# Optimization experiments

Measured on AMD Instinct MI355X. Metric: run time of the kernel, lower is better.

Reference implementation:

```python
import jax, jax.numpy as jnp
import numpy as np

EPS = 1e-6

def setup_inputs() -> dict:
    key = jax.random.key(0)
    ks = jax.random.split(key, 12)
    B, C, H, W = 2, 192, 192, 192
    f = lambda k, s, sc=1.0: jax.random.normal(k, s, dtype=jnp.float32) * sc
    d = {}
    d["x_l"] = f(ks[0], (B, C, H, W))
    d["x_r"] = f(ks[1], (B, C, H, W))
    d["ln_l_w"] = jnp.ones((C,), jnp.float32)
    d["ln_l_b"] = jnp.zeros((C,), jnp.float32)
    d["ln_r_w"] = jnp.ones((C,), jnp.float32)
    d["ln_r_b"] = jnp.zeros((C,), jnp.float32)
    s = C ** -0.5
    d["wq_l"] = f(ks[2], (C, C), s)   # 1x1 conv weights as [out,in]
    d["wq_r"] = f(ks[3], (C, C), s)
    d["wv_l"] = f(ks[4], (C, C), s)
    d["wv_r"] = f(ks[5], (C, C), s)
    d["mlp_w1"] = f(ks[6], (C // 24, C // 3), (C // 3) ** -0.5)
    d["mlp_w2"] = f(ks[7], (C * 2 // 3, C // 24), (C // 24) ** -0.5)
    d["scale_h"] = jnp.ones((1,), jnp.float32)
    d["scale_w"] = jnp.ones((1,), jnp.float32)
    # layer scales are zero-init in the module; use small random so output is nontrivial
    d["ls1"] = f(ks[8], (1, C, 1, 1), 0.1)
    d["ls2"] = f(ks[9], (1, C, 1, 1), 0.1)
    return d

def _ln2d(x, w, b):
    # LayerNorm over channel dim of NCHW
    mu = x.mean(1, keepdims=True)
    var = ((x - mu) ** 2).mean(1, keepdims=True)
    return (x - mu) * jax.lax.rsqrt(var + EPS) * w[None, :, None, None] + b[None, :, None, None]

def _pw(x, w):
    # 1x1 conv, no bias
    return jnp.einsum('bchw,oc->bohw', x, w)

def reference(x_l, x_r, ln_l_w, ln_l_b, ln_r_w, ln_r_b, wq_l, wq_r, wv_l, wv_r,
              mlp_w1, mlp_w2, scale_h, scale_w, ls1, ls2):
    q_l_h, q_l_w, q_l_c = jnp.split(_pw(_ln2d(x_l, ln_l_w, ln_l_b), wq_l), 3, axis=1)
    q_r_h, q_r_w, q_r_c = jnp.split(_pw(_ln2d(x_r, ln_r_w, ln_r_b), wq_r), 3, axis=1)
    v_l_h, v_l_w, v_l_c = jnp.split(_pw(x_l, wv_l), 3, axis=1)
    v_r_h, v_r_w, v_r_c = jnp.split(_pw(x_r, wv_r), 3, axis=1)

    # height axial attention: scores [b, w, h, h']
    attn_h = jnp.einsum('bchw,bcgw->bwhg', q_l_h, q_r_h) * scale_h[0]
    attn_h = jax.nn.softmax(attn_h, axis=-1)
    x_r2l_h = jnp.einsum('bwhg,bcgw->bchw', attn_h, v_r_h)           # [b,c,h,w]
    x_l2r_h = jnp.einsum('bwhg,bchw->bcgw', attn_h, v_l_h)           # attn^T @ v_l

    # width axial attention: scores [b, h, w, w'] (softmax applied separately per direction)
    attn_w = jnp.einsum('bchw,bchv->bhwv', q_l_w, q_r_w) * scale_w[0]
    a1 = jax.nn.softmax(attn_w, axis=-1)
    x_r2l_w = jnp.einsum('bhwv,bchv->bchw', a1, v_r_w)
    a2 = jax.nn.softmax(jnp.swapaxes(attn_w, -1, -2), axis=-1)       # [b,h,v,w]
    x_l2r_w = jnp.einsum('bhvw,bchw->bchv', a2, v_l_w)

    # channel SE branch: sum of the two channel queries, GAP, bottleneck MLP
    p = (q_l_c + q_r_c).mean(axis=(2, 3))                            # [b, c]
    h1 = jax.nn.relu(p @ mlp_w1.T)                                   # [b, c//8]
    a = jax.nn.softmax(h1 @ mlp_w2.T, axis=1)                        # softmax over 2c channels jointly
    attn_l_c, attn_r_c = jnp.split(a, 2, axis=1)
    x_r2l_c = attn_l_c[:, :, None, None] * v_l_c
    x_l2r_c = attn_r_c[:, :, None, None] * v_r_c

    x_r2l = jnp.concatenate([x_r2l_h, x_r2l_w, x_r2l_c], axis=1)
    x_l2r = jnp.concatenate([x_l2r_h, x_l2r_w, x_l2r_c], axis=1)
    out_l = x_r2l * ls1 + x_l
    out_r = x_l2r * ls2 + x_r
    return (out_l, out_r)
```

## Files before the change

kernel.cpp:

```cpp
#include <hip/hip_runtime.h>
#include <stdint.h>

#define NN 36864
#define PL 7077888
#define PL64 2359296
#define TOT 14155776

typedef unsigned short ushort_t;
typedef __attribute__((ext_vector_type(8))) __bf16 bf16x8;
typedef __attribute__((ext_vector_type(4))) float f32x4;
typedef __attribute__((ext_vector_type(4))) unsigned int u32x4;
typedef __attribute__((ext_vector_type(2))) unsigned int u32x2;

__device__ __forceinline__ ushort_t f2bf(float f) {
  unsigned int u = __builtin_bit_cast(unsigned int, f);
  u = (u + 0x7FFFu + ((u >> 16) & 1u)) >> 16;
  return (ushort_t)u;
}
__device__ __forceinline__ float bf2f(ushort_t h) {
  unsigned int u = ((unsigned int)h) << 16;
  return __builtin_bit_cast(float, u);
}
__device__ __forceinline__ bf16x8 lds8(const ushort_t* p) {
  return __builtin_bit_cast(bf16x8, *(const u32x4*)p);
}
__device__ __forceinline__ f32x4 mfma16(bf16x8 a, bf16x8 b, f32x4 c) {
  return __builtin_amdgcn_mfma_f32_16x16x32_bf16(a, b, c, 0, 0, 0);
}
__device__ __forceinline__ unsigned cvtpk(float lo, float hi) {
  unsigned r;
  asm("v_cvt_pk_bf16_f32 %0, %1, %2" : "=v"(r) : "v"(lo), "v"(hi));
  return r;
}

__global__ void k_prep(const float* __restrict__ wq, const float* __restrict__ wv,
                       const float* __restrict__ lnw, const float* __restrict__ lnb,
                       ushort_t* __restrict__ W, float* __restrict__ ab) {
  __shared__ float sa[3], sb[3];
  int r = blockIdx.x, t = threadIdx.x;
  if (r < 192) {
    float w  = wq[r*192 + t];
    float lw = lnw[t], lb = lnb[t];
    W[r*192 + t] = f2bf(w * lw);
    float av = w * lb, bv = -w * lw;
    #pragma unroll
    for (int off = 1; off < 64; off <<= 1) {
      av += __shfl_xor(av, off);
      bv += __shfl_xor(bv, off);
    }
    if ((t & 63) == 0) { sa[t >> 6] = av; sb[t >> 6] = bv; }
    __syncthreads();
    if (t == 0) { ab[r] = sa[0]+sa[1]+sa[2]; ab[192 + r] = sb[0]+sb[1]+sb[2]; }
  } else {
    W[r*192 + t] = f2bf(wv[(r-192)*192 + t]);
  }
}

__global__ __launch_bounds__(512, 2) void k_proj(
    const float* __restrict__ xl, const float* __restrict__ xr,
    const ushort_t* __restrict__ Wl, const ushort_t* __restrict__ Wr,
    const float* __restrict__ abl, const float* __restrict__ abr,
    ushort_t* __restrict__ qhTl, ushort_t* __restrict__ qhTr,
    ushort_t* __restrict__ qwTl, ushort_t* __restrict__ qwTr,
    ushort_t* __restrict__ Vl, ushort_t* __restrict__ Vr,
    float* __restrict__ gpart) {
  __shared__ union {
    struct { ushort_t A[2][4096]; ushort_t B[2][6144]; } kl;
    struct { ushort_t T[192*72]; float gsum[64]; } ep;
  } sm;
  __shared__ float spart[4][192], spart2[4][192];
  __shared__ float smu[192], srs[192];

  const int side = blockIdx.y;
  const float*    x  = side ? xr  : xl;
  const ushort_t* W  = side ? Wr  : Wl;
  const float*    ab = side ? abr : abl;
  ushort_t* qhT = side ? qhTr : qhTl;
  ushort_t* qwT = side ? qwTr : qwTl;
  ushort_t* V   = side ? Vr   : Vl;

  const int bx = blockIdx.x;
  const int mb = bx % 3;
  const int bh = bx / 3;
  const int b  = bh / 192, h = bh % 192;
  const int m0 = mb * 128;
  const int tid = threadIdx.x;
  const int wave = tid >> 6, lane = tid & 63, lr = lane & 15, lg = lane >> 4;
  const int wm = wave >> 2, wn = wave & 3;

  const int kg0 = tid / 192, n_0 = tid - kg0 * 192;
  const int id1 = 512 + (tid & 255);
  const int kg1 = id1 / 192, n_1 = id1 - kg1 * 192;
  const float* xb0 = x + (size_t)b*PL + (size_t)(kg0*8)*NN + h*192 + n_0;
  const float* xb1 = x + (size_t)b*PL + (size_t)(kg1*8)*NN + h*192 + n_1;
  const int bw0 = n_0*32 + 8*(kg0 ^ ((n_0 >> 1) & 3));
  const int bw1 = n_1*32 + 8*(kg1 ^ ((n_1 >> 1) & 3));
  const int am = tid >> 2, akb = tid & 3;
  const ushort_t* wsrc = W + (m0 + am)*192 + akb*8;
  const int aw = am*32 + 8*(akb ^ ((am >> 1) & 3));
  const int slotR = 8 * (lg ^ ((lr >> 1) & 3));

  const f32x4 fz = {0.f, 0.f, 0.f, 0.f};
  f32x4 acc[4][3];
  #pragma unroll
  for (int mf = 0; mf < 4; ++mf)
    #pragma unroll
    for (int nf = 0; nf < 3; ++nf) acc[mf][nf] = fz;

  float sA0 = 0.f, sB0 = 0.f, sA1 = 0.f, sB1 = 0.f;

  {
    u32x4 aV = *(const u32x4*)wsrc;
    float g0[8], g1[8];
    #pragma unroll
    for (int j = 0; j < 8; ++j) g0[j] = xb0[(size_t)j*NN];
    if (tid < 256) {
      #pragma unroll
      for (int j = 0; j < 8; ++j) g1[j] = xb1[(size_t)j*NN];
    }
    *(u32x4*)&sm.kl.A[0][aw] = aV;
    union { ushort_t us[8]; u32x4 v; } t0;
    #pragma unroll
    for (int j = 0; j < 8; ++j) { t0.us[j] = f2bf(g0[j]); sA0 += g0[j]; sB0 += g0[j]*g0[j]; }
    *(u32x4*)&sm.kl.B[0][bw0] = t0.v;
    if (tid < 256) {
      union { ushort_t us[8]; u32x4 v; } t1;
      #pragma unroll
      for (int j = 0; j < 8; ++j) { t1.us[j] = f2bf(g1[j]); sA1 += g1[j]; sB1 += g1[j]*g1[j]; }
      *(u32x4*)&sm.kl.B[0][bw1] = t1.v;
    }
  }
  __syncthreads();

  for (int ks = 0; ks < 6; ++ks) {
    const int cur = ks & 1, nxt = cur ^ 1;
    u32x4 aN;
    float g0[8], g1[8];
    if (ks < 5) {
      const int k0n = (ks + 1) * 32;
      aN = *(const u32x4*)(wsrc + k0n);
      #pragma unroll
      for (int j = 0; j < 8; ++j) g0[j] = xb0[(size_t)(k0n + j)*NN];
      if (tid < 256) {
        #pragma unroll
        for (int j = 0; j < 8; ++j) g1[j] = xb1[(size_t)(k0n + j)*NN];
      }
    }
    bf16x8 bfr[3];
    #pragma unroll
    for (int nf = 0; nf < 3; ++nf)
      bfr[nf] = lds8(&sm.kl.B[cur][(wn*48 + nf*16 + lr)*32 + slotR]);
    #pragma unroll
    for (int mf = 0; mf < 4; ++mf) {
      bf16x8 af = lds8(&sm.kl.A[cur][(wm*64 + mf*16 + lr)*32 + slotR]);
      #pragma unroll
      for (int nf = 0; nf < 3; ++nf) acc[mf][nf] = mfma16(af, bfr[nf], acc[mf][nf]);
    }
    if (ks < 5) {
      *(u32x4*)&sm.kl.A[nxt][aw] = aN;
      union { ushort_t us[8]; u32x4 v; } t0;
      #pragma unroll
      for (int j = 0; j < 8; ++j) { t0.us[j] = f2bf(g0[j]); sA0 += g0[j]; sB0 += g0[j]*g0[j]; }
      *(u32x4*)&sm.kl.B[nxt][bw0] = t0.v;
      if (tid < 256) {
        union { ushort_t us[8]; u32x4 v; } t1;
        #pragma unroll
        for (int j = 0; j < 8; ++j) { t1.us[j] = f2bf(g1[j]); sA1 += g1[j]; sB1 += g1[j]*g1[j]; }
        *(u32x4*)&sm.kl.B[nxt][bw1] = t1.v;
      }
    }
    __syncthreads();
  }

  spart[kg0][n_0] = sA0; spart2[kg0][n_0] = sB0;
  if (tid < 256) { spart[kg1][n_1] = sA1; spart2[kg1][n_1] = sB1; }
  if (mb == 1 && tid >= 448) sm.ep.gsum[tid - 448] = 0.f;
  __syncthreads();
  if (tid < 192) {
    float s  = spart[0][tid] + spart[1][tid] + spart[2][tid] + spart[3][tid];
    float s2 = spart2[0][tid] + spart2[1][tid] + spart2[2][tid] + spart2[3][tid];
    float mu = s * (1.f/192.f);
    float var = s2 * (1.f/192.f) - mu*mu;
    smu[tid] = mu;
    srs[tid] = rsqrtf(var + 1e-6f);
  }
  __syncthreads();

  if (mb == 0) {
    float rst[3], mrs[3];
    #pragma unroll
    for (int nf = 0; nf < 3; ++nf) {
      int n_ = wn*48 + nf*16 + lr;
      float rs = srs[n_];
      rst[nf] = rs;
      mrs[nf] = smu[n_] * rs;
    }
    #pragma unroll
    for (int mf = 0; mf < 4; ++mf) {
      #pragma unroll
      for (int i = 0; i < 4; ++i) {
        int m = wm*64 + mf*16 + lg*4 + i;
        float a_ = ab[m], bb = ab[192 + m];
        #pragma unroll
        for (int nf = 0; nf < 3; ++nf)
          acc[mf][nf][i] = acc[mf][nf][i]*rst[nf] + bb*mrs[nf] + a_;
      }
    }
    if (wm == 0) {
      #pragma unroll
      for (int mf = 0; mf < 4; ++mf)
        #pragma unroll
        for (int nf = 0; nf < 3; ++nf)
          #pragma unroll
          for (int i = 0; i < 4; ++i)
            sm.ep.T[(wn*48 + nf*16 + lr)*72 + mf*16 + lg*4 + i] = f2bf(acc[mf][nf][i]);
    }
    __syncthreads();
    #pragma unroll
    for (int p = 0; p < 3; ++p) {
      int id = p*512 + tid, n = id >> 3, c8 = id & 7;
      u32x4 v = *(const u32x4*)&sm.ep.T[n*72 + c8*8];
      *(u32x4*)&qhT[(((size_t)b*192 + n)*192 + h)*64 + c8*8] = v;
    }
    __syncthreads();
    if (wm == 1) {
      #pragma unroll
      for (int mf = 0; mf < 4; ++mf)
        #pragma unroll
        for (int nf = 0; nf < 3; ++nf)
          #pragma unroll
          for (int i = 0; i < 4; ++i)
            sm.ep.T[(wn*48 + nf*16 + lr)*72 + mf*16 + lg*4 + i] = f2bf(acc[mf][nf][i]);
    }
    __syncthreads();
    #pragma unroll
    for (int p = 0; p < 3; ++p) {
      int id = p*512 + tid, n = id >> 3, c8 = id & 7;
      u32x4 v = *(const u32x4*)&sm.ep.T[n*72 + c8*8];
      *(u32x4*)&qwT[(((size_t)b*192 + h)*192 + n)*64 + c8*8] = v;
    }
  } else {
    if (mb == 1) {
      if (wm == 0) {
        float rst[3], mrs[3];
        #pragma unroll
        for (int nf = 0; nf < 3; ++nf) {
          int n_ = wn*48 + nf*16 + lr;
          float rs = srs[n_];
          rst[nf] = rs;
          mrs[nf] = smu[n_] * rs;
        }
        #pragma unroll
        for (int mf = 0; mf < 4; ++mf) {
          #pragma unroll
          for (int i = 0; i < 4; ++i) {
            int m = 128 + mf*16 + lg*4 + i;
            float a_ = ab[m], bb = ab[192 + m];
            float part = 0.f;
            #pragma unroll
            for (int nf = 0; nf < 3; ++nf)
              part += acc[mf][nf][i]*rst[nf] + bb*mrs[nf] + a_;
            #pragma unroll
            for (int off = 1; off < 16; off <<= 1) part += __shfl_xor(part, off);
            if (lr == 0) atomicAdd(&sm.ep.gsum[mf*16 + lg*4 + i], part);
          }
        }
      } else {
        #pragma unroll
        for (int mf = 0; mf < 4; ++mf)
          #pragma unroll
          for (int i = 0; i < 4; ++i) {
            int c = mf*16 + lg*4 + i;
            #pragma unroll
            for (int nf = 0; nf < 3; ++nf)
              V[((size_t)b*192 + c)*NN + h*192 + wn*48 + nf*16 + lr] = f2bf(acc[mf][nf][i]);
          }
      }
      __syncthreads();
      if (tid < 64) gpart[(((size_t)side*2 + b)*192 + h)*64 + tid] = sm.ep.gsum[tid];
    } else {
      #pragma unroll
      for (int mf = 0; mf < 4; ++mf)
        #pragma unroll
        for (int i = 0; i < 4; ++i) {
          int c = 64 + wm*64 + mf*16 + lg*4 + i;
          #pragma unroll
          for (int nf = 0; nf < 3; ++nf)
            V[((size_t)b*192 + c)*NN + h*192 + wn*48 + nf*16 + lr] = f2bf(acc[mf][nf][i]);
        }
    }
  }
}

__global__ void k_repack_v(const ushort_t* __restrict__ Vl, const ushort_t* __restrict__ Vr,
                           ushort_t* __restrict__ vhTl, ushort_t* __restrict__ vhTr) {
  __shared__ ushort_t Ls[64*72];
  const ushort_t* V = blockIdx.y ? Vr : Vl;
  ushort_t* out = blockIdx.y ? vhTr : vhTl;
  int bx = blockIdx.x;
  int b = bx / 576, rem = bx % 576;
  int c = rem / 9, tt = rem % 9;
  int h0 = (tt/3)*64, w0 = (tt%3)*64;
  int tid = threadIdx.x;
  #pragma unroll
  for (int i = 0; i < 2; ++i) {
    int idx = tid + 256*i;
    int hh = idx >> 3, wb = idx & 7;
    *(u32x4*)&Ls[hh*72 + wb*8] =
      *(const u32x4*)&V[(size_t)(b*192 + c)*NN + (h0+hh)*192 + w0 + wb*8];
  }
  __syncthreads();
  #pragma unroll
  for (int i = 0; i < 2; ++i) {
    int idx = tid + 256*i;
    int ww = idx >> 3, hb = idx & 7;
    union { ushort_t us[8]; u32x4 v; } tu;
    #pragma unroll
    for (int j = 0; j < 8; ++j) tu.us[j] = Ls[(hb*8+j)*72 + ww];
    *(u32x4*)&out[(size_t)(b*64 + c)*NN + (w0+ww)*192 + h0 + hb*8] = tu.v;
  }
}

__global__ __launch_bounds__(256, 2) void k_attn(
    const ushort_t* __restrict__ qhTl, const ushort_t* __restrict__ qhTr,
    const ushort_t* __restrict__ qwTl, const ushort_t* __restrict__ qwTr,
    const ushort_t* __restrict__ Vl,  const ushort_t* __restrict__ Vr,
    const ushort_t* __restrict__ vhTl, const ushort_t* __restrict__ vhTr,
    const float* __restrict__ sch, const float* __restrict__ scw,
    ushort_t* __restrict__ Oh1, ushort_t* __restrict__ Oh2,
    ushort_t* __restrict__ Ow1, ushort_t* __restrict__ Ow2) {
  __shared__ ushort_t Qsl[192*64];
  __shared__ ushort_t Qsr[192*64];
  __shared__ ushort_t Vs[64*192];
  __shared__ float md[192*2];

  const int tid = threadIdx.x;
  const int wave = tid >> 6, lane = tid & 63, lr = lane & 15, lg = lane >> 4;
  const int bx = blockIdx.x;
  const int mode = bx / 384;
  const int b = (bx % 384) / 192, s0 = bx % 192;
  const float scl = (mode ? scw : sch)[0];

  const ushort_t* ql = (mode ? qwTl : qhTl) + (size_t)(b*192 + s0)*12288;
  const ushort_t* qr = (mode ? qwTr : qhTr) + (size_t)(b*192 + s0)*12288;
  const ushort_t* vr = mode ? Vr + (size_t)(b*192 + 64)*NN + s0*192
                            : vhTr + (size_t)b*PL64 + s0*192;
  const ushort_t* vl = mode ? Vl + (size_t)(b*192 + 64)*NN + s0*192
                            : vhTl + (size_t)b*PL64 + s0*192;
  ushort_t* og1 = (mode ? Ow1 : Oh1) + (size_t)(b*192 + s0)*12288;
  ushort_t* og2 = (mode ? Ow2 : Oh2) + (size_t)(b*192 + s0)*12288;

  #pragma unroll
  for (int i = 0; i < 6; ++i) {
    int idx = tid + 256*i;
    int r = idx >> 3, sl = idx & 7;
    int dq = r*64 + ((sl ^ (r & 7)) << 3);
    *(u32x4*)&Qsl[dq] = *(const u32x4*)&ql[idx*8];
    *(u32x4*)&Qsr[dq] = *(const u32x4*)&qr[idx*8];
    int c = idx / 24, gs = idx % 24;
    *(u32x4*)&Vs[c*192 + ((gs ^ (c & 7)) << 3)] = *(const u32x4*)&vr[(size_t)c*NN + gs*8];
  }
  __syncthreads();

  const f32x4 fz = {0.f, 0.f, 0.f, 0.f};
  f32x4 acc[12][3];
  unsigned pk[3][12][2];

  auto qk = [&](bool swap) {
    const ushort_t* A  = swap ? Qsl : Qsr;
    const ushort_t* Bq = swap ? Qsr : Qsl;
    #pragma unroll
    for (int mf = 0; mf < 12; ++mf)
      #pragma unroll
      for (int nf = 0; nf < 3; ++nf) acc[mf][nf] = fz;
    __builtin_amdgcn_s_setprio(1);
    #pragma unroll
    for (int kh = 0; kh < 2; ++kh) {
      bf16x8 bq[3];
      #pragma unroll
      for (int nf = 0; nf < 3; ++nf) {
        int r = wave*48 + nf*16 + lr;
        bq[nf] = lds8(&Bq[r*64 + (((kh*4 + lg) ^ (r & 7)) << 3)]);
      }
      #pragma unroll
      for (int mf = 0; mf < 12; ++mf) {
        int r = mf*16 + lr;
        bf16x8 aq = lds8(&A[r*64 + (((kh*4 + lg) ^ (r & 7)) << 3)]);
        #pragma unroll
        for (int nf = 0; nf < 3; ++nf) acc[mf][nf] = mfma16(aq, bq[nf], acc[mf][nf]);
      }
    }
    __builtin_amdgcn_s_setprio(0);
  };

  auto smpack = [&](bool store_md) {
    #pragma unroll
    for (int nf = 0; nf < 3; ++nf) {
      float mx = -3.4e38f;
      #pragma unroll
      for (int mf = 0; mf < 12; ++mf)
        #pragma unroll
        for (int i = 0; i < 4; ++i) {
          float v = acc[mf][nf][i] * scl;
          acc[mf][nf][i] = v;
          mx = fmaxf(mx, v);
        }
      mx = fmaxf(mx, __shfl_xor(mx, 16));
      mx = fmaxf(mx, __shfl_xor(mx, 32));
      float den = 0.f;
      #pragma unroll
      for (int mf = 0; mf < 12; ++mf)
        #pragma unroll
        for (int i = 0; i < 4; ++i) {
          float e = __expf(acc[mf][nf][i] - mx);
          acc[mf][nf][i] = e;
          den += e;
        }
      den += __shfl_xor(den, 16);
      den += __shfl_xor(den, 32);
      float rd = 1.f / den;
      if (store_md && lg == 0) {
        int col = wave*48 + nf*16 + lr;
        md[col*2] = mx; md[col*2+1] = rd;
      }
      #pragma unroll
      for (int mf = 0; mf < 12; ++mf) {
        pk[nf][mf][0] = cvtpk(acc[mf][nf][0]*rd, acc[mf][nf][1]*rd);
        pk[nf][mf][1] = cvtpk(acc[mf][nf][2]*rd, acc[mf][nf][3]*rd);
      }
    }
  };

  auto pv = [&](unsigned obf[4][3][2]) {
    f32x4 o[4][3];
    #pragma unroll
    for (int mf = 0; mf < 4; ++mf)
      #pragma unroll
      for (int nf = 0; nf < 3; ++nf) o[mf][nf] = fz;
    const int sA = lr + 32*(lg & 1), sB = sA + 16;
    const bool hi = (lg >> 1) != 0;
    __builtin_amdgcn_s_setprio(1);
    #pragma unroll
    for (int ks = 0; ks < 6; ++ks) {
      bf16x8 av[4];
      #pragma unroll
      for (int mf = 0; mf < 4; ++mf) {
        int c = mf*16 + lr;
        av[mf] = lds8(&Vs[c*192 + (((4*ks + lg) ^ (c & 7)) << 3)]);
      }
      #pragma unroll
      for (int nf = 0; nf < 3; ++nf) {
        unsigned w0a = (unsigned)__shfl((int)pk[nf][2*ks  ][0], sA);
        unsigned w0b = (unsigned)__shfl((int)pk[nf][2*ks+1][0], sA);
        unsigned w1a = (unsigned)__shfl((int)pk[nf][2*ks  ][1], sA);
        unsigned w1b = (unsigned)__shfl((int)pk[nf][2*ks+1][1], sA);
        unsigned w2a = (unsigned)__shfl((int)pk[nf][2*ks  ][0], sB);
        unsigned w2b = (unsigned)__shfl((int)pk[nf][2*ks+1][0], sB);
        unsigned w3a = (unsigned)__shfl((int)pk[nf][2*ks  ][1], sB);
        unsigned w3b = (unsigned)__shfl((int)pk[nf][2*ks+1][1], sB);
        u32x4 wv = { hi ? w0b : w0a, hi ? w1b : w1a, hi ? w2b : w2a, hi ? w3b : w3a };
        bf16x8 bp = __builtin_bit_cast(bf16x8, wv);
        #pragma unroll
        for (int mf = 0; mf < 4; ++mf) o[mf][nf] = mfma16(av[mf], bp, o[mf][nf]);
      }
    }
    __builtin_amdgcn_s_setprio(0);
    #pragma unroll
    for (int mf = 0; mf < 4; ++mf)
      #pragma unroll
      for (int nf = 0; nf < 3; ++nf) {
        obf[mf][nf][0] = cvtpk(o[mf][nf][0], o[mf][nf][1]);
        obf[mf][nf][1] = cvtpk(o[mf][nf][2], o[mf][nf][3]);
      }
  };

  auto owrite = [&](unsigned obf[4][3][2]) {
    char* Ot = (char*)Qsl;
    #pragma unroll
    for (int mf = 0; mf < 4; ++mf)
      #pragma unroll
      for (int nf = 0; nf < 3; ++nf) {
        int col = wave*48 + nf*16 + lr;
        int byte = col*128 + ((mf*32 + lg*8) ^ ((col & 7) << 4));
        u32x2 v = { obf[mf][nf][0], obf[mf][nf][1] };
        *(u32x2*)(Ot + byte) = v;
      }
  };

  auto ostore = [&](ushort_t* og) {
    const char* Ot = (const char*)Qsl;
    #pragma unroll
    for (int it = 0; it < 6; ++it) {
      int id = tid + 256*it;
      int col = id >> 3, s = id & 7;
      int byte = col*128 + ((s*16) ^ ((col & 7) << 4));
      u32x4 v = *(const u32x4*)(Ot + byte);
      *(u32x4*)&og[(size_t)col*64 + s*8] = v;
    }
  };

  qk(false);
  smpack(true);
  unsigned o1bf[4][3][2];
  pv(o1bf);

  u32x4 vlr[6];
  #pragma unroll
  for (int i = 0; i < 6; ++i) {
    int idx = tid + 256*i;
    int c = idx / 24, gs = idx % 24;
    vlr[i] = *(const u32x4*)&vl[(size_t)c*NN + gs*8];
  }

  qk(true);
  __syncthreads();

  owrite(o1bf);
  #pragma unroll
  for (int i = 0; i < 6; ++i) {
    int idx = tid + 256*i;
    int c = idx / 24, gs = idx % 24;
    *(u32x4*)&Vs[c*192 + ((gs ^ (c & 7)) << 3)] = vlr[i];
  }

  if (mode == 0) {
    #pragma unroll
    for (int mf = 0; mf < 12; ++mf)
      #pragma unroll
      for (int i = 0; i < 4; ++i) {
        int row = mf*16 + lg*4 + i;
        float m_ = md[row*2], rd_ = md[row*2+1];
        #pragma unroll
        for (int nf = 0; nf < 3; ++nf)
          acc[mf][nf][i] = __expf(acc[mf][nf][i]*scl - m_) * rd_;
      }
    #pragma unroll
    for (int nf = 0; nf < 3; ++nf)
      #pragma unroll
      for (int mf = 0; mf < 12; ++mf) {
        pk[nf][mf][0] = cvtpk(acc[mf][nf][0], acc[mf][nf][1]);
        pk[nf][mf][1] = cvtpk(acc[mf][nf][2], acc[mf][nf][3]);
      }
  } else {
    smpack(false);
  }
  __syncthreads();

  ostore(og1);
  unsigned o2bf[4][3][2];
  pv(o2bf);
  __syncthreads();
  owrite(o2bf);
  __syncthreads();
  ostore(og2);
}

__global__ void k_se(const float* __restrict__ gpart, const float* __restrict__ w1,
                     const float* __restrict__ w2, float* __restrict__ sea) {
  __shared__ float p[2][64];
  __shared__ float h1[2][8];
  __shared__ float lgt[2][128];
  __shared__ float mred[2], dred[2];
  int t = threadIdx.x;
  if (t < 128) {
    int b = t >> 6, c = t & 63;
    float s = 0.f;
    for (int side = 0; side < 2; ++side)
      for (int h = 0; h < 192; ++h)
        s += gpart[(((size_t)side*2 + b)*192 + h)*64 + c];
    p[b][c] = s * (1.f/36864.f);
  }
  __syncthreads();
  if (t < 16) {
    int bb = t >> 3, j = t & 7;
    float s = 0.f;
    for (int k = 0; k < 64; ++k) s += p[bb][k] * w1[j*64 + k];
    h1[bb][j] = fmaxf(s, 0.f);
  }
  __syncthreads();
  {
    int bb = t >> 7, o = t & 127;
    float s = 0.f;
    #pragma unroll
    for (int j = 0; j < 8; ++j) s += h1[bb][j] * w2[o*8 + j];
    lgt[bb][o] = s;
  }
  __syncthreads();
  if (t < 2) {
    float mx = -3.4e38f;
    for (int o = 0; o < 128; ++o) mx = fmaxf(mx, lgt[t][o]);
    float d = 0.f;
    for (int o = 0; o < 128; ++o) d += __expf(lgt[t][o] - mx);
    mred[t] = mx; dred[t] = d;
  }
  __syncthreads();
  {
    int bb = t >> 7, o = t & 127;
    sea[bb*128 + o] = __expf(lgt[bb][o] - mred[bb]) / dred[bb];
  }
}

__global__ __launch_bounds__(256, 4) void k_ep(
    const ushort_t* __restrict__ Oh1, const ushort_t* __restrict__ Oh2,
    const ushort_t* __restrict__ Ow1, const ushort_t* __restrict__ Ow2,
    const ushort_t* __restrict__ Vl, const ushort_t* __restrict__ Vr,
    const float* __restrict__ sea,
    const float* __restrict__ xl, const float* __restrict__ xr,
    const float* __restrict__ ls1, const float* __restrict__ ls2,
    float* __restrict__ out) {
  __shared__ ushort_t T[192*64];
  const int gid = blockIdx.x;
  const int h = gid % 192;
  const int b = (gid / 192) % 2;
  const int dir = gid / 384;
  const int tid = threadIdx.x;
  const float* xin = dir ? xr : xl;
  const float* ls  = dir ? ls2 : ls1;
  const ushort_t* Oh = dir ? Oh2 : Oh1;
  const ushort_t* Ow = dir ? Ow2 : Ow1;
  const ushort_t* Vv = dir ? Vr  : Vl;
  float* outp = out + (size_t)dir*TOT;

  const int c0 = (tid / 24) * 8, wseg = tid % 24, w0 = wseg * 8;
  const int Srd = (wseg & 7) << 4;

  auto flush = [&](int cbase) {
    if (tid < 192) {
      u32x4 r[8];
      #pragma unroll
      for (int j = 0; j < 8; ++j)
        r[j] = *(const u32x4*)((const char*)T + (w0 + j)*128 + ((c0*2) ^ Srd));
      #pragma unroll
      for (int k = 0; k < 8; ++k) {
        int c = cbase + c0 + k;
        float lsv = ls[c];
        size_t oo = (size_t)(b*192 + c)*NN + h*192 + w0;
        f32x4 xa = *(const f32x4*)&xin[oo];
        f32x4 xb2 = *(const f32x4*)&xin[oo + 4];
        f32x4 r0, r1;
        #pragma unroll
        for (int j = 0; j < 4; ++j) r0[j] = bf2f(((const ushort_t*)&r[j])[k])*lsv + xa[j];
        #pragma unroll
        for (int j = 0; j < 4; ++j) r1[j] = bf2f(((const ushort_t*)&r[4+j])[k])*lsv + xb2[j];
        *(f32x4*)&outp[oo] = r0;
        *(f32x4*)&outp[oo + 4] = r1;
      }
    }
  };

  {
    const ushort_t* ohb = Oh + ((size_t)b*192*192 + h)*64;
    #pragma unroll
    for (int it = 0; it < 6; ++it) {
      int id = tid + 256*it;
      int w = id >> 3, s = id & 7;
      u32x4 v = *(const u32x4*)&ohb[(size_t)w*12288 + s*8];
      *(u32x4*)((char*)T + w*128 + ((s*16) ^ (((w >> 3) & 7) << 4))) = v;
    }
  }
  __syncthreads();
  flush(0);
  __syncthreads();

  {
    const ushort_t* owb = Ow + ((size_t)b*192 + h)*12288;
    #pragma unroll
    for (int it = 0; it < 6; ++it) {
      int id = tid + 256*it;
      int w = id >> 3, s = id & 7;
      u32x4 v = *(const u32x4*)&owb[id*8];
      *(u32x4*)((char*)T + w*128 + ((s*16) ^ (((w >> 3) & 7) << 4))) = v;
    }
  }
  __syncthreads();
  flush(64);

  #pragma unroll
  for (int it = 0; it < 6; ++it) {
    int id = tid + 256*it;
    int cc = id / 24, ws = (id % 24) * 8;
    float lsv = ls[128 + cc] * sea[b*128 + dir*64 + cc];
    size_t oo = (size_t)(b*192 + 128 + cc)*NN + h*192 + ws;
    u32x4 sv = *(const u32x4*)&Vv[(size_t)(b*192 + 128 + cc)*NN + h*192 + ws];
    const ushort_t* sp = (const ushort_t*)&sv;
    f32x4 xa = *(const f32x4*)&xin[oo];
    f32x4 xb2 = *(const f32x4*)&xin[oo + 4];
    f32x4 r0, r1;
    #pragma unroll
    for (int j = 0; j < 4; ++j) r0[j] = bf2f(sp[j])*lsv + xa[j];
    #pragma unroll
    for (int j = 0; j < 4; ++j) r1[j] = bf2f(sp[4+j])*lsv + xb2[j];
    *(f32x4*)&outp[oo] = r0;
    *(f32x4*)&outp[oo + 4] = r1;
  }
}

extern "C" void kernel_launch(void* const* d_in, const int* in_sizes, int n_in,
                              void* d_out, int out_size, void* d_ws, size_t ws_size,
                              hipStream_t stream) {
  const float* x_l  = (const float*)d_in[0];
  const float* x_r  = (const float*)d_in[1];
  const float* lnlw = (const float*)d_in[2];
  const float* lnlb = (const float*)d_in[3];
  const float* lnrw = (const float*)d_in[4];
  const float* lnrb = (const float*)d_in[5];
  const float* wq_l = (const float*)d_in[6];
  const float* wq_r = (const float*)d_in[7];
  const float* wv_l = (const float*)d_in[8];
  const float* wv_r = (const float*)d_in[9];
  const float* w1   = (const float*)d_in[10];
  const float* w2   = (const float*)d_in[11];
  const float* sch  = (const float*)d_in[12];
  const float* scw  = (const float*)d_in[13];
  const float* ls1  = (const float*)d_in[14];
  const float* ls2  = (const float*)d_in[15];
  float* out = (float*)d_out;

  char* ws = (char*)d_ws;
  size_t off = 0;
  auto alloc = [&](size_t bytes) {
    char* p = ws + off;
    off += (bytes + 255) & ~(size_t)255;
    return p;
  };
  ushort_t* Vl   = (ushort_t*)alloc((size_t)2*192*NN*2);
  ushort_t* Vr   = (ushort_t*)alloc((size_t)2*192*NN*2);
  ushort_t* qhTl = (ushort_t*)alloc((size_t)2*64*NN*2);
  ushort_t* qhTr = (ushort_t*)alloc((size_t)2*64*NN*2);
  ushort_t* qwTl = (ushort_t*)alloc((size_t)2*64*NN*2);
  ushort_t* qwTr = (ushort_t*)alloc((size_t)2*64*NN*2);
  ushort_t* vhTl = (ushort_t*)alloc((size_t)2*64*NN*2);
  ushort_t* vhTr = (ushort_t*)alloc((size_t)2*64*NN*2);
  ushort_t* Oh1  = (ushort_t*)alloc((size_t)2*64*NN*2);
  ushort_t* Oh2  = (ushort_t*)alloc((size_t)2*64*NN*2);
  ushort_t* Ow1  = (ushort_t*)alloc((size_t)2*64*NN*2);
  ushort_t* Ow2  = (ushort_t*)alloc((size_t)2*64*NN*2);
  ushort_t* Wl   = (ushort_t*)alloc((size_t)384*192*2);
  ushort_t* Wr   = (ushort_t*)alloc((size_t)384*192*2);
  float* abl = (float*)alloc(384*4);
  float* abr = (float*)alloc(384*4);
  float* gpart = (float*)alloc((size_t)2*2*192*64*4);
  float* sea = (float*)alloc(2*128*4);
  (void)in_sizes; (void)n_in; (void)out_size; (void)ws_size;

  k_prep<<<384, 192, 0, stream>>>(wq_l, wv_l, lnlw, lnlb, Wl, abl);
  k_prep<<<384, 192, 0, stream>>>(wq_r, wv_r, lnrw, lnrb, Wr, abr);
  k_proj<<<dim3(1152, 2), 512, 0, stream>>>(x_l, x_r, Wl, Wr, abl, abr,
                                            qhTl, qhTr, qwTl, qwTr, Vl, Vr, gpart);
  k_repack_v<<<dim3(1152, 2), 256, 0, stream>>>(Vl, Vr, vhTl, vhTr);
  k_attn<<<768, 256, 0, stream>>>(qhTl, qhTr, qwTl, qwTr, Vl, Vr, vhTl, vhTr,
                                  sch, scw, Oh1, Oh2, Ow1, Ow2);
  k_se<<<1, 256, 0, stream>>>(gpart, w1, w2, sea);
  k_ep<<<768, 256, 0, stream>>>(Oh1, Oh2, Ow1, Ow2, Vl, Vr, sea,
                                x_l, x_r, ls1, ls2, out);
}
```

Before: 246.0 us.

## Compute all projection outputs per row in one block, reading x once

The projection kernel now uses one block per (batch, row) that computes all 384 output channels, instead of three blocks that each reloaded and bf16-converted the same x tile and recomputed LayerNorm statistics. Weight fragments are read directly from global memory (likely L2-resident) rather than staged through LDS. V outputs are now staged through LDS so their global stores are coalesced. The trade-off is a much larger per-thread accumulator (12x3 MFMA tiles), which under the 512-thread, 2-blocks-per-CU launch bound risks register spilling or lower occupancy, plus one third as many blocks.

Result: slower. 280.6 us (+14.0%).

```diff
diff --git a/kernel.cpp b/kernel.cpp
--- a/kernel.cpp
+++ b/kernel.cpp
@@ -65,11 +65,13 @@
     ushort_t* __restrict__ Vl, ushort_t* __restrict__ Vr,
     float* __restrict__ gpart) {
   __shared__ union {
-    struct { ushort_t A[2][4096]; ushort_t B[2][6144]; } kl;
-    struct { ushort_t T[192*72]; float gsum[64]; } ep;
+    ushort_t B[2][6144];
+    ushort_t T[13824];
+    ushort_t Tv[12800];
   } sm;
   __shared__ float spart[4][192], spart2[4][192];
   __shared__ float smu[192], srs[192];
+  __shared__ float gsum[64];
 
   const int side = blockIdx.y;
   const float*    x  = side ? xr  : xl;
@@ -79,11 +81,8 @@
   ushort_t* qwT = side ? qwTr : qwTl;
   ushort_t* V   = side ? Vr   : Vl;
 
-  const int bx = blockIdx.x;
-  const int mb = bx % 3;
-  const int bh = bx / 3;
+  const int bh = blockIdx.x;
   const int b  = bh / 192, h = bh % 192;
-  const int m0 = mb * 128;
   const int tid = threadIdx.x;
   const int wave = tid >> 6, lane = tid & 63, lr = lane & 15, lg = lane >> 4;
   const int wm = wave >> 2, wn = wave & 3;
@@ -95,22 +94,21 @@
   const float* xb1 = x + (size_t)b*PL + (size_t)(kg1*8)*NN + h*192 + n_1;
   const int bw0 = n_0*32 + 8*(kg0 ^ ((n_0 >> 1) & 3));
   const int bw1 = n_1*32 + 8*(kg1 ^ ((n_1 >> 1) & 3));
-  const int am = tid >> 2, akb = tid & 3;
-  const ushort_t* wsrc = W + (m0 + am)*192 + akb*8;
-  const int aw = am*32 + 8*(akb ^ ((am >> 1) & 3));
   const int slotR = 8 * (lg ^ ((lr >> 1) & 3));
+  const ushort_t* wbase = W + ((size_t)(wm*192 + lr))*192 + lg*8;
+
+  if (tid < 64) gsum[tid] = 0.f;
 
   const f32x4 fz = {0.f, 0.f, 0.f, 0.f};
-  f32x4 acc[4][3];
-  #pragma unroll
-  for (int mf = 0; mf < 4; ++mf)
+  f32x4 acc[12][3];
+  #pragma unroll
+  for (int mf = 0; mf < 12; ++mf)
     #pragma unroll
     for (int nf = 0; nf < 3; ++nf) acc[mf][nf] = fz;
 
   float sA0 = 0.f, sB0 = 0.f, sA1 = 0.f, sB1 = 0.f;
 
   {
-    u32x4 aV = *(const u32x4*)wsrc;
     float g0[8], g1[8];
     #pragma unroll
     for (int j = 0; j < 8; ++j) g0[j] = xb0[(size_t)j*NN];
@@ -118,27 +116,24 @@
       #pragma unroll
       for (int j = 0; j < 8; ++j) g1[j] = xb1[(size_t)j*NN];
     }
-    *(u32x4*)&sm.kl.A[0][aw] = aV;
     union { ushort_t us[8]; u32x4 v; } t0;
     #pragma unroll
     for (int j = 0; j < 8; ++j) { t0.us[j] = f2bf(g0[j]); sA0 += g0[j]; sB0 += g0[j]*g0[j]; }
-    *(u32x4*)&sm.kl.B[0][bw0] = t0.v;
+    *(u32x4*)&sm.B[0][bw0] = t0.v;
     if (tid < 256) {
       union { ushort_t us[8]; u32x4 v; } t1;
       #pragma unroll
       for (int j = 0; j < 8; ++j) { t1.us[j] = f2bf(g1[j]); sA1 += g1[j]; sB1 += g1[j]*g1[j]; }
-      *(u32x4*)&sm.kl.B[0][bw1] = t1.v;
+      *(u32x4*)&sm.B[0][bw1] = t1.v;
     }
   }
   __syncthreads();
 
   for (int ks = 0; ks < 6; ++ks) {
     const int cur = ks & 1, nxt = cur ^ 1;
-    u32x4 aN;
     float g0[8], g1[8];
     if (ks < 5) {
       const int k0n = (ks + 1) * 32;
-      aN = *(const u32x4*)(wsrc + k0n);
       #pragma unroll
       for (int j = 0; j < 8; ++j) g0[j] = xb0[(size_t)(k0n + j)*NN];
       if (tid < 256) {
@@ -149,24 +144,26 @@
     bf16x8 bfr[3];
     #pragma unroll
     for (int nf = 0; nf < 3; ++nf)
-      bfr[nf] = lds8(&sm.kl.B[cur][(wn*48 + nf*16 + lr)*32 + slotR]);
-    #pragma unroll
-    for (int mf = 0; mf < 4; ++mf) {
-      bf16x8 af = lds8(&sm.kl.A[cur][(wm*64 + mf*16 + lr)*32 + slotR]);
-      #pragma unroll
-      for (int nf = 0; nf < 3; ++nf) acc[mf][nf] = mfma16(af, bfr[nf], acc[mf][nf]);
+      bfr[nf] = lds8(&sm.B[cur][(wn*48 + nf*16 + lr)*32 + slotR]);
+    bf16x8 afr[12];
+    #pragma unroll
+    for (int mf = 0; mf < 12; ++mf)
+      afr[mf] = lds8(wbase + mf*3072 + ks*32);
+    #pragma unroll
+    for (int mf = 0; mf < 12; ++mf) {
+      #pragma unroll
+      for (int nf = 0; nf < 3; ++nf) acc[mf][nf] = mfma16(afr[mf], bfr[nf], acc[mf][nf]);
     }
     if (ks < 5) {
-      *(u32x4*)&sm.kl.A[nxt][aw] = aN;
       union { ushort_t us[8]; u32x4 v; } t0;
       #pragma unroll
       for (int j = 0; j < 8; ++j) { t0.us[j] = f2bf(g0[j]); sA0 += g0[j]; sB0 += g0[j]*g0[j]; }
-      *(u32x4*)&sm.kl.B[nxt][bw0] = t0.v;
+      *(u32x4*)&sm.B[nxt][bw0] = t0.v;
       if (tid < 256) {
         union { ushort_t us[8]; u32x4 v; } t1;
         #pragma unroll
         for (int j = 0; j < 8; ++j) { t1.us[j] = f2bf(g1[j]); sA1 += g1[j]; sB1 += g1[j]*g1[j]; }
-        *(u32x4*)&sm.kl.B[nxt][bw1] = t1.v;
+        *(u32x4*)&sm.B[nxt][bw1] = t1.v;
       }
     }
     __syncthreads();
@@ -174,7 +171,6 @@
 
   spart[kg0][n_0] = sA0; spart2[kg0][n_0] = sB0;
   if (tid < 256) { spart[kg1][n_1] = sA1; spart2[kg1][n_1] = sB1; }
-  if (mb == 1 && tid >= 448) sm.ep.gsum[tid - 448] = 0.f;
   __syncthreads();
   if (tid < 192) {
     float s  = spart[0][tid] + spart[1][tid] + spart[2][tid] + spart[3][tid];
@@ -186,7 +182,7 @@
   }
   __syncthreads();
 
-  if (mb == 0) {
+  if (wm == 0) {
     float rst[3], mrs[3];
     #pragma unroll
     for (int nf = 0; nf < 3; ++nf) {
@@ -196,98 +192,89 @@
       mrs[nf] = smu[n_] * rs;
     }
     #pragma unroll
-    for (int mf = 0; mf < 4; ++mf) {
+    for (int mf = 0; mf < 12; ++mf) {
       #pragma unroll
       for (int i = 0; i < 4; ++i) {
-        int m = wm*64 + mf*16 + lg*4 + i;
+        int m = mf*16 + lg*4 + i;
         float a_ = ab[m], bb = ab[192 + m];
         #pragma unroll
         for (int nf = 0; nf < 3; ++nf)
           acc[mf][nf][i] = acc[mf][nf][i]*rst[nf] + bb*mrs[nf] + a_;
       }
     }
-    if (wm == 0) {
-      #pragma unroll
-      for (int mf = 0; mf < 4; ++mf)
+  }
+
+  if (wm == 0) {
+    #pragma unroll
+    for (int mf = 0; mf < 4; ++mf)
+      #pragma unroll
+      for (int nf = 0; nf < 3; ++nf)
+        #pragma unroll
+        for (int i = 0; i < 4; ++i)
+          sm.T[(wn*48 + nf*16 + lr)*72 + mf*16 + lg*4 + i] = f2bf(acc[mf][nf][i]);
+  }
+  __syncthreads();
+  #pragma unroll
+  for (int p = 0; p < 3; ++p) {
+    int id = p*512 + tid, n = id >> 3, c8 = id & 7;
+    u32x4 v = *(const u32x4*)&sm.T[n*72 + c8*8];
+    *(u32x4*)&qhT[(((size_t)b*192 + n)*192 + h)*64 + c8*8] = v;
+  }
+  __syncthreads();
+
+  if (wm == 0) {
+    #pragma unroll
+    for (int mf = 4; mf < 8; ++mf)
+      #pragma unroll
+      for (int nf = 0; nf < 3; ++nf)
+        #pragma unroll
+        for (int i = 0; i < 4; ++i)
+          sm.T[(wn*48 + nf*16 + lr)*72 + (mf-4)*16 + lg*4 + i] = f2bf(acc[mf][nf][i]);
+  }
+  __syncthreads();
+  #pragma unroll
+  for (int p = 0; p < 3; ++p) {
+    int id = p*512 + tid, n = id >> 3, c8 = id & 7;
+    u32x4 v = *(const u32x4*)&sm.T[n*72 + c8*8];
+    *(u32x4*)&qwT[(((size_t)b*192 + h)*192 + n)*64 + c8*8] = v;
+  }
+
+  if (wm == 0) {
+    #pragma unroll
+    for (int mf = 8; mf < 12; ++mf) {
+      #pragma unroll
+      for (int i = 0; i < 4; ++i) {
+        float part = acc[mf][0][i] + acc[mf][1][i] + acc[mf][2][i];
+        #pragma unroll
+        for (int off = 1; off < 16; off <<= 1) part += __shfl_xor(part, off);
+        if (lr == 0) atomicAdd(&gsum[(mf-8)*16 + lg*4 + i], part);
+      }
+    }
+  }
+  __syncthreads();
+  if (tid < 64) gpart[(((size_t)side*2 + b)*192 + h)*64 + tid] = gsum[tid];
+
+  #pragma unroll
+  for (int ch = 0; ch < 3; ++ch) {
+    __syncthreads();
+    if (wm == 1) {
+      #pragma unroll
+      for (int q = 0; q < 4; ++q) {
+        int mf = ch*4 + q;
         #pragma unroll
         for (int nf = 0; nf < 3; ++nf)
           #pragma unroll
           for (int i = 0; i < 4; ++i)
-            sm.ep.T[(wn*48 + nf*16 + lr)*72 + mf*16 + lg*4 + i] = f2bf(acc[mf][nf][i]);
+            sm.Tv[(q*16 + lg*4 + i)*200 + wn*48 + nf*16 + lr] = f2bf(acc[mf][nf][i]);
+      }
     }
     __syncthreads();
     #pragma unroll
     for (int p = 0; p < 3; ++p) {
-      int id = p*512 + tid, n = id >> 3, c8 = id & 7;
-      u32x4 v = *(const u32x4*)&sm.ep.T[n*72 + c8*8];
-      *(u32x4*)&qhT[(((size_t)b*192 + n)*192 + h)*64 + c8*8] = v;
-    }
-    __syncthreads();
-    if (wm == 1) {
-      #pragma unroll
-      for (int mf = 0; mf < 4; ++mf)
-        #pragma unroll
-        for (int nf = 0; nf < 3; ++nf)
-          #pragma unroll
-          for (int i = 0; i < 4; ++i)
-            sm.ep.T[(wn*48 + nf*16 + lr)*72 + mf*16 + lg*4 + i] = f2bf(acc[mf][nf][i]);
-    }
-    __syncthreads();
-    #pragma unroll
-    for (int p = 0; p < 3; ++p) {
-      int id = p*512 + tid, n = id >> 3, c8 = id & 7;
-      u32x4 v = *(const u32x4*)&sm.ep.T[n*72 + c8*8];
-      *(u32x4*)&qwT[(((size_t)b*192 + h)*192 + n)*64 + c8*8] = v;
-    }
-  } else {
-    if (mb == 1) {
-      if (wm == 0) {
-        float rst[3], mrs[3];
-        #pragma unroll
-        for (int nf = 0; nf < 3; ++nf) {
-          int n_ = wn*48 + nf*16 + lr;
-          float rs = srs[n_];
-          rst[nf] = rs;
-          mrs[nf] = smu[n_] * rs;
-        }
-        #pragma unroll
-        for (int mf = 0; mf < 4; ++mf) {
-          #pragma unroll
-          for (int i = 0; i < 4; ++i) {
-            int m = 128 + mf*16 + lg*4 + i;
-            float a_ = ab[m], bb = ab[192 + m];
-            float part = 0.f;
-            #pragma unroll
-            for (int nf = 0; nf < 3; ++nf)
-              part += acc[mf][nf][i]*rst[nf] + bb*mrs[nf] + a_;
-            #pragma unroll
-            for (int off = 1; off < 16; off <<= 1) part += __shfl_xor(part, off);
-            if (lr == 0) atomicAdd(&sm.ep.gsum[mf*16 + lg*4 + i], part);
-          }
-        }
-      } else {
-        #pragma unroll
-        for (int mf = 0; mf < 4; ++mf)
-          #pragma unroll
-          for (int i = 0; i < 4; ++i) {
-            int c = mf*16 + lg*4 + i;
-            #pragma unroll
-            for (int nf = 0; nf < 3; ++nf)
-              V[((size_t)b*192 + c)*NN + h*192 + wn*48 + nf*16 + lr] = f2bf(acc[mf][nf][i]);
-          }
-      }
-      __syncthreads();
-      if (tid < 64) gpart[(((size_t)side*2 + b)*192 + h)*64 + tid] = sm.ep.gsum[tid];
-    } else {
-      #pragma unroll
-      for (int mf = 0; mf < 4; ++mf)
-        #pragma unroll
-        for (int i = 0; i < 4; ++i) {
-          int c = 64 + wm*64 + mf*16 + lg*4 + i;
-          #pragma unroll
-          for (int nf = 0; nf < 3; ++nf)
-            V[((size_t)b*192 + c)*NN + h*192 + wn*48 + nf*16 + lr] = f2bf(acc[mf][nf][i]);
-        }
+      int id = p*512 + tid;
+      int cc = id / 24, seg = id % 24;
+      u32x4 v = *(const u32x4*)&sm.Tv[cc*200 + seg*8];
+      *(u32x4*)&V[((size_t)b*192 + ch*64 + cc)*NN + h*192 + seg*8] = v;
     }
   }
 }
@@ -745,8 +732,8 @@
 
   k_prep<<<384, 192, 0, stream>>>(wq_l, wv_l, lnlw, lnlb, Wl, abl);
   k_prep<<<384, 192, 0, stream>>>(wq_r, wv_r, lnrw, lnrb, Wr, abr);
-  k_proj<<<dim3(1152, 2), 512, 0, stream>>>(x_l, x_r, Wl, Wr, abl, abr,
-                                            qhTl, qhTr, qwTl, qwTr, Vl, Vr, gpart);
+  k_proj<<<dim3(384, 2), 512, 0, stream>>>(x_l, x_r, Wl, Wr, abl, abr,
+                                           qhTl, qhTr, qwTl, qwTr, Vl, Vr, gpart);
   k_repack_v<<<dim3(1152, 2), 256, 0, stream>>>(Vl, Vr, vhTl, vhTr);
   k_attn<<<768, 256, 0, stream>>>(qhTl, qhTr, qwTl, qwTr, Vl, Vr, vhTl, vhTr,
                                   sch, scw, Oh1, Oh2, Ow1, Ow2);
```

## Stage V projection stores through LDS and remap k_proj blocks for occupancy

Applied to the files above, without the earlier changes.

V outputs of the projection kernel are now written to a padded LDS tile and then stored as 16-byte coalesced row segments, replacing the scattered 2-byte global stores. The grid is flattened and remapped so consecutive blocks cover 8 rows across both sides and all three m-blocks, which should improve L2 reuse of x. Launch bounds are raised to 4 blocks per CU. The mb==2 path adds extra barriers for its two-pass staging, and the tighter register budget could cause spills.

Result: slower. 329.7 us (+34.0%).

```diff
diff --git a/kernel.cpp b/kernel.cpp
--- a/kernel.cpp
+++ b/kernel.cpp
@@ -56,7 +56,7 @@
   }
 }
 
-__global__ __launch_bounds__(512, 2) void k_proj(
+__global__ __launch_bounds__(512, 4) void k_proj(
     const float* __restrict__ xl, const float* __restrict__ xr,
     const ushort_t* __restrict__ Wl, const ushort_t* __restrict__ Wr,
     const float* __restrict__ abl, const float* __restrict__ abr,
@@ -66,12 +66,21 @@
     float* __restrict__ gpart) {
   __shared__ union {
     struct { ushort_t A[2][4096]; ushort_t B[2][6144]; } kl;
-    struct { ushort_t T[192*72]; float gsum[64]; } ep;
+    struct { ushort_t T[13824]; } ep;
+    struct { ushort_t Tv[12800]; } tv;
   } sm;
   __shared__ float spart[4][192], spart2[4][192];
   __shared__ float smu[192], srs[192];
-
-  const int side = blockIdx.y;
+  __shared__ float gsum[64];
+
+  const int bx = blockIdx.x;
+  const int g = bx / 48, rr = bx % 48;
+  const int bh = g*8 + (rr & 7);
+  const int ms = rr >> 3;
+  const int mb = ms >> 1, side = ms & 1;
+  const int b  = bh / 192, h = bh % 192;
+  const int m0 = mb * 128;
+
   const float*    x  = side ? xr  : xl;
   const ushort_t* W  = side ? Wr  : Wl;
   const float*    ab = side ? abr : abl;
@@ -79,11 +88,6 @@
   ushort_t* qwT = side ? qwTr : qwTl;
   ushort_t* V   = side ? Vr   : Vl;
 
-  const int bx = blockIdx.x;
-  const int mb = bx % 3;
-  const int bh = bx / 3;
-  const int b  = bh / 192, h = bh % 192;
-  const int m0 = mb * 128;
   const int tid = threadIdx.x;
   const int wave = tid >> 6, lane = tid & 63, lr = lane & 15, lg = lane >> 4;
   const int wm = wave >> 2, wn = wave & 3;
@@ -100,6 +104,8 @@
   const int aw = am*32 + 8*(akb ^ ((am >> 1) & 3));
   const int slotR = 8 * (lg ^ ((lr >> 1) & 3));
 
+  if (tid < 64) gsum[tid] = 0.f;
+
   const f32x4 fz = {0.f, 0.f, 0.f, 0.f};
   f32x4 acc[4][3];
   #pragma unroll
@@ -174,7 +180,6 @@
 
   spart[kg0][n_0] = sA0; spart2[kg0][n_0] = sB0;
   if (tid < 256) { spart[kg1][n_1] = sA1; spart2[kg1][n_1] = sB1; }
-  if (mb == 1 && tid >= 448) sm.ep.gsum[tid - 448] = 0.f;
   __syncthreads();
   if (tid < 192) {
     float s  = spart[0][tid] + spart[1][tid] + spart[2][tid] + spart[3][tid];
@@ -239,55 +244,70 @@
       u32x4 v = *(const u32x4*)&sm.ep.T[n*72 + c8*8];
       *(u32x4*)&qwT[(((size_t)b*192 + h)*192 + n)*64 + c8*8] = v;
     }
+  } else if (mb == 1) {
+    if (wm == 0) {
+      float rst[3], mrs[3];
+      #pragma unroll
+      for (int nf = 0; nf < 3; ++nf) {
+        int n_ = wn*48 + nf*16 + lr;
+        float rs = srs[n_];
+        rst[nf] = rs;
+        mrs[nf] = smu[n_] * rs;
+      }
+      #pragma unroll
+      for (int mf = 0; mf < 4; ++mf) {
+        #pragma unroll
+        for (int i = 0; i < 4; ++i) {
+          int m = 128 + mf*16 + lg*4 + i;
+          float a_ = ab[m], bb = ab[192 + m];
+          float part = 0.f;
+          #pragma unroll
+          for (int nf = 0; nf < 3; ++nf)
+            part += acc[mf][nf][i]*rst[nf] + bb*mrs[nf] + a_;
+          #pragma unroll
+          for (int off = 1; off < 16; off <<= 1) part += __shfl_xor(part, off);
+          if (lr == 0) atomicAdd(&gsum[mf*16 + lg*4 + i], part);
+        }
+      }
+    } else {
+      #pragma unroll
+      for (int mf = 0; mf < 4; ++mf)
+        #pragma unroll
+        for (int nf = 0; nf < 3; ++nf)
+          #pragma unroll
+          for (int i = 0; i < 4; ++i)
+            sm.tv.Tv[(mf*16 + lg*4 + i)*200 + wn*48 + nf*16 + lr] = f2bf(acc[mf][nf][i]);
+    }
+    __syncthreads();
+    if (tid < 64) gpart[(((size_t)side*2 + b)*192 + h)*64 + tid] = gsum[tid];
+    #pragma unroll
+    for (int p = 0; p < 3; ++p) {
+      int id = p*512 + tid;
+      int cc = id / 24, seg = id % 24;
+      u32x4 v = *(const u32x4*)&sm.tv.Tv[cc*200 + seg*8];
+      *(u32x4*)&V[((size_t)b*192 + cc)*NN + h*192 + seg*8] = v;
+    }
   } else {
-    if (mb == 1) {
-      if (wm == 0) {
-        float rst[3], mrs[3];
-        #pragma unroll
-        for (int nf = 0; nf < 3; ++nf) {
-          int n_ = wn*48 + nf*16 + lr;
-          float rs = srs[n_];
-          rst[nf] = rs;
-          mrs[nf] = smu[n_] * rs;
-        }
-        #pragma unroll
-        for (int mf = 0; mf < 4; ++mf) {
-          #pragma unroll
-          for (int i = 0; i < 4; ++i) {
-            int m = 128 + mf*16 + lg*4 + i;
-            float a_ = ab[m], bb = ab[192 + m];
-            float part = 0.f;
-            #pragma unroll
-            for (int nf = 0; nf < 3; ++nf)
-              part += acc[mf][nf][i]*rst[nf] + bb*mrs[nf] + a_;
-            #pragma unroll
-            for (int off = 1; off < 16; off <<= 1) part += __shfl_xor(part, off);
-            if (lr == 0) atomicAdd(&sm.ep.gsum[mf*16 + lg*4 + i], part);
-          }
-        }
-      } else {
+    #pragma unroll
+    for (int ch = 0; ch < 2; ++ch) {
+      if (wm == ch) {
         #pragma unroll
         for (int mf = 0; mf < 4; ++mf)
           #pragma unroll
-          for (int i = 0; i < 4; ++i) {
-            int c = mf*16 + lg*4 + i;
+          for (int nf = 0; nf < 3; ++nf)
             #pragma unroll
-            for (int nf = 0; nf < 3; ++nf)
-              V[((size_t)b*192 + c)*NN + h*192 + wn*48 + nf*16 + lr] = f2bf(acc[mf][nf][i]);
-          }
+            for (int i = 0; i < 4; ++i)
+              sm.tv.Tv[(mf*16 + lg*4 + i)*200 + wn*48 + nf*16 + lr] = f2bf(acc[mf][nf][i]);
       }
       __syncthreads();
-      if (tid < 64) gpart[(((size_t)side*2 + b)*192 + h)*64 + tid] = sm.ep.gsum[tid];
-    } else {
-      #pragma unroll
-      for (int mf = 0; mf < 4; ++mf)
-        #pragma unroll
-        for (int i = 0; i < 4; ++i) {
-          int c = 64 + wm*64 + mf*16 + lg*4 + i;
-          #pragma unroll
-          for (int nf = 0; nf < 3; ++nf)
-            V[((size_t)b*192 + c)*NN + h*192 + wn*48 + nf*16 + lr] = f2bf(acc[mf][nf][i]);
-        }
+      #pragma unroll
+      for (int p = 0; p < 3; ++p) {
+        int id = p*512 + tid;
+        int cc = id / 24, seg = id % 24;
+        u32x4 v = *(const u32x4*)&sm.tv.Tv[cc*200 + seg*8];
+        *(u32x4*)&V[((size_t)b*192 + 64 + ch*64 + cc)*NN + h*192 + seg*8] = v;
+      }
+      __syncthreads();
     }
   }
 }
@@ -745,8 +765,8 @@
 
   k_prep<<<384, 192, 0, stream>>>(wq_l, wv_l, lnlw, lnlb, Wl, abl);
   k_prep<<<384, 192, 0, stream>>>(wq_r, wv_r, lnrw, lnrb, Wr, abr);
-  k_proj<<<dim3(1152, 2), 512, 0, stream>>>(x_l, x_r, Wl, Wr, abl, abr,
-                                            qhTl, qhTr, qwTl, qwTr, Vl, Vr, gpart);
+  k_proj<<<2304, 512, 0, stream>>>(x_l, x_r, Wl, Wr, abl, abr,
+                                   qhTl, qhTr, qwTl, qwTr, Vl, Vr, gpart);
   k_repack_v<<<dim3(1152, 2), 256, 0, stream>>>(Vl, Vr, vhTl, vhTr);
   k_attn<<<768, 256, 0, stream>>>(qhTl, qhTr, qwTl, qwTr, Vl, Vr, vhTl, vhTr,
                                   sch, scw, Oh1, Oh2, Ow1, Ow2);
```

## Split LayerNorm statistics into separate kernel and raise k_proj occupancy

Applied to the files above, without the earlier changes.

Computes per-pixel channel mean and rstd in a new k_stats kernel that reads both inputs once, and drops the in-loop sum/sumsq accumulation and shared-memory reduction from k_proj. k_proj now reads the precomputed stats from global memory in its epilogue, which frees registers and LDS, and its launch bounds are raised to 4 blocks per SM. The trade-off is an extra full pass over x_l and x_r (about 113 MB) plus one more kernel launch, in exchange for a lighter, higher-occupancy projection GEMM.

Result: faster. 239.5 us (-2.6%).

```diff
diff --git a/kernel.cpp b/kernel.cpp
--- a/kernel.cpp
+++ b/kernel.cpp
@@ -56,10 +56,29 @@
   }
 }
 
-__global__ __launch_bounds__(512, 2) void k_proj(
+__global__ void k_stats(const float* __restrict__ xl, const float* __restrict__ xr,
+                        float* __restrict__ stl, float* __restrict__ str) {
+  int bid = blockIdx.x;
+  int side = bid / 288, rem = bid % 288;
+  int b = rem / 144, nb = rem % 144;
+  const float* x = side ? xr : xl;
+  float* st = side ? str : stl;
+  int n = nb*256 + threadIdx.x;
+  const float* p = x + (size_t)b*PL + n;
+  float s = 0.f, s2 = 0.f;
+  #pragma unroll 4
+  for (int c = 0; c < 192; ++c) { float v = p[(size_t)c*NN]; s += v; s2 += v*v; }
+  float mu = s * (1.f/192.f);
+  float var = s2 * (1.f/192.f) - mu*mu;
+  st[(b*2+0)*NN + n] = mu;
+  st[(b*2+1)*NN + n] = rsqrtf(var + 1e-6f);
+}
+
+__global__ __launch_bounds__(512, 4) void k_proj(
     const float* __restrict__ xl, const float* __restrict__ xr,
     const ushort_t* __restrict__ Wl, const ushort_t* __restrict__ Wr,
     const float* __restrict__ abl, const float* __restrict__ abr,
+    const float* __restrict__ stl, const float* __restrict__ str,
     ushort_t* __restrict__ qhTl, ushort_t* __restrict__ qhTr,
     ushort_t* __restrict__ qwTl, ushort_t* __restrict__ qwTr,
     ushort_t* __restrict__ Vl, ushort_t* __restrict__ Vr,
@@ -68,13 +87,12 @@
     struct { ushort_t A[2][4096]; ushort_t B[2][6144]; } kl;
     struct { ushort_t T[192*72]; float gsum[64]; } ep;
   } sm;
-  __shared__ float spart[4][192], spart2[4][192];
-  __shared__ float smu[192], srs[192];
 
   const int side = blockIdx.y;
   const float*    x  = side ? xr  : xl;
   const ushort_t* W  = side ? Wr  : Wl;
   const float*    ab = side ? abr : abl;
+  const float*    st = side ? str : stl;
   ushort_t* qhT = side ? qhTr : qhTl;
   ushort_t* qwT = side ? qwTr : qwTl;
   ushort_t* V   = side ? Vr   : Vl;
@@ -107,8 +125,6 @@
     #pragma unroll
     for (int nf = 0; nf < 3; ++nf) acc[mf][nf] = fz;
 
-  float sA0 = 0.f, sB0 = 0.f, sA1 = 0.f, sB1 = 0.f;
-
   {
     u32x4 aV = *(const u32x4*)wsrc;
     float g0[8], g1[8];
@@ -121,12 +137,12 @@
     *(u32x4*)&sm.kl.A[0][aw] = aV;
     union { ushort_t us[8]; u32x4 v; } t0;
     #pragma unroll
-    for (int j = 0; j < 8; ++j) { t0.us[j] = f2bf(g0[j]); sA0 += g0[j]; sB0 += g0[j]*g0[j]; }
+    for (int j = 0; j < 8; ++j) t0.us[j] = f2bf(g0[j]);
     *(u32x4*)&sm.kl.B[0][bw0] = t0.v;
     if (tid < 256) {
       union { ushort_t us[8]; u32x4 v; } t1;
       #pragma unroll
-      for (int j = 0; j < 8; ++j) { t1.us[j] = f2bf(g1[j]); sA1 += g1[j]; sB1 += g1[j]*g1[j]; }
+      for (int j = 0; j < 8; ++j) t1.us[j] = f2bf(g1[j]);
       *(u32x4*)&sm.kl.B[0][bw1] = t1.v;
     }
   }
@@ -160,40 +176,26 @@
       *(u32x4*)&sm.kl.A[nxt][aw] = aN;
       union { ushort_t us[8]; u32x4 v; } t0;
       #pragma unroll
-      for (int j = 0; j < 8; ++j) { t0.us[j] = f2bf(g0[j]); sA0 += g0[j]; sB0 += g0[j]*g0[j]; }
+      for (int j = 0; j < 8; ++j) t0.us[j] = f2bf(g0[j]);
       *(u32x4*)&sm.kl.B[nxt][bw0] = t0.v;
       if (tid < 256) {
         union { ushort_t us[8]; u32x4 v; } t1;
         #pragma unroll
-        for (int j = 0; j < 8; ++j) { t1.us[j] = f2bf(g1[j]); sA1 += g1[j]; sB1 += g1[j]*g1[j]; }
+        for (int j = 0; j < 8; ++j) t1.us[j] = f2bf(g1[j]);
         *(u32x4*)&sm.kl.B[nxt][bw1] = t1.v;
       }
     }
     __syncthreads();
   }
-
-  spart[kg0][n_0] = sA0; spart2[kg0][n_0] = sB0;
-  if (tid < 256) { spart[kg1][n_1] = sA1; spart2[kg1][n_1] = sB1; }
-  if (mb == 1 && tid >= 448) sm.ep.gsum[tid - 448] = 0.f;
-  __syncthreads();
-  if (tid < 192) {
-    float s  = spart[0][tid] + spart[1][tid] + spart[2][tid] + spart[3][tid];
-    float s2 = spart2[0][tid] + spart2[1][tid] + spart2[2][tid] + spart2[3][tid];
-    float mu = s * (1.f/192.f);
-    float var = s2 * (1.f/192.f) - mu*mu;
-    smu[tid] = mu;
-    srs[tid] = rsqrtf(var + 1e-6f);
-  }
-  __syncthreads();
 
   if (mb == 0) {
     float rst[3], mrs[3];
     #pragma unroll
     for (int nf = 0; nf < 3; ++nf) {
-      int n_ = wn*48 + nf*16 + lr;
-      float rs = srs[n_];
+      int n_ = h*192 + wn*48 + nf*16 + lr;
+      float rs = st[(b*2+1)*NN + n_];
       rst[nf] = rs;
-      mrs[nf] = smu[n_] * rs;
+      mrs[nf] = st[(b*2+0)*NN + n_] * rs;
     }
     #pragma unroll
     for (int mf = 0; mf < 4; ++mf) {
@@ -240,15 +242,17 @@
       *(u32x4*)&qwT[(((size_t)b*192 + h)*192 + n)*64 + c8*8] = v;
     }
   } else {
+    if (mb == 1 && tid < 64) sm.ep.gsum[tid] = 0.f;
+    __syncthreads();
     if (mb == 1) {
       if (wm == 0) {
         float rst[3], mrs[3];
         #pragma unroll
         for (int nf = 0; nf < 3; ++nf) {
-          int n_ = wn*48 + nf*16 + lr;
-          float rs = srs[n_];
+          int n_ = h*192 + wn*48 + nf*16 + lr;
+          float rs = st[(b*2+1)*NN + n_];
           rst[nf] = rs;
-          mrs[nf] = smu[n_] * rs;
+          mrs[nf] = st[(b*2+0)*NN + n_] * rs;
         }
         #pragma unroll
         for (int mf = 0; mf < 4; ++mf) {
@@ -739,13 +743,16 @@
   ushort_t* Wr   = (ushort_t*)alloc((size_t)384*192*2);
   float* abl = (float*)alloc(384*4);
   float* abr = (float*)alloc(384*4);
+  float* stl = (float*)alloc((size_t)4*NN*4);
+  float* str = (float*)alloc((size_t)4*NN*4);
   float* gpart = (float*)alloc((size_t)2*2*192*64*4);
   float* sea = (float*)alloc(2*128*4);
   (void)in_sizes; (void)n_in; (void)out_size; (void)ws_size;
 
   k_prep<<<384, 192, 0, stream>>>(wq_l, wv_l, lnlw, lnlb, Wl, abl);
   k_prep<<<384, 192, 0, stream>>>(wq_r, wv_r, lnrw, lnrb, Wr, abr);
-  k_proj<<<dim3(1152, 2), 512, 0, stream>>>(x_l, x_r, Wl, Wr, abl, abr,
+  k_stats<<<576, 256, 0, stream>>>(x_l, x_r, stl, str);
+  k_proj<<<dim3(1152, 2), 512, 0, stream>>>(x_l, x_r, Wl, Wr, abl, abr, stl, str,
                                             qhTl, qhTr, qwTl, qwTr, Vl, Vr, gpart);
   k_repack_v<<<dim3(1152, 2), 256, 0, stream>>>(Vl, Vr, vhTl, vhTr);
   k_attn<<<768, 256, 0, stream>>>(qhTl, qhTr, qwTl, qwTr, Vl, Vr, vhTl, vhTr,
```
